# Kernel tuning notes

Measured on AMD Instinct MI355X. Metric: run time of the kernel, lower is better.

## Reference

```python
import jax, jax.numpy as jnp
import numpy as np

RADIUS = 5
KERNEL = 2 * RADIUS + 1  # 11
N_PATCHES = KERNEL * KERNEL  # 121
SIGMA_DIAG = np.array([10.0, 10.0, 0.02, 0.02, 0.02, 0.1, 0.1, 0.1], dtype=np.float32)


def _shift(x):
    # x: [B, C, H, W] -> [B, P, C, H, W] with P = KERNEL^2 reflect-padded window shifts
    b, c, h, w = x.shape
    xp = jnp.pad(x, ((0, 0), (0, 0), (RADIUS, RADIUS), (RADIUS, RADIUS)), mode='reflect')
    patches = [xp[:, :, dy:dy + h, dx:dx + w]
               for dy in range(KERNEL) for dx in range(KERNEL)]
    return jnp.stack(patches, axis=1)


def setup_inputs() -> dict:
    key = jax.random.key(0)
    k1, k2 = jax.random.split(key)
    image = jax.random.uniform(k1, (2, 3, 256, 256), dtype=jnp.float32)
    guidance = jax.random.uniform(k2, (2, 8, 256, 256), dtype=jnp.float32)
    return {"image": image, "guidance": guidance}


def reference(image, guidance):
    # sigma_inv = inverse of diag(SIGMA_DIAG): diagonal, so just reciprocal per channel
    sigma_inv = jnp.asarray(1.0 / SIGMA_DIAG, dtype=guidance.dtype)  # [8]

    sg = _shift(guidance)                       # [B, P, 8, H, W]
    center = sg[:, N_PATCHES // 2:N_PATCHES // 2 + 1]
    diff = sg - center                          # [B, P, 8, H, W]
    # Mahalanobis^2 with diagonal sigma_inv: sum_c diff^2 / sigma_c
    maha_sq = jnp.einsum('bpchw,c->bphw', diff * diff, sigma_inv)
    weights = jnp.exp(-0.5 * maha_sq)           # [B, P, H, W]

    si = _shift(image)                          # [B, P, 3, H, W]
    weighted_sum = jnp.einsum('bpchw,bphw->bchw', si, weights)
    sum_w = jnp.clip(jnp.sum(weights, axis=1, keepdims=False), 1e-10, None)  # [B, H, W]
    return weighted_sum / sum_w[:, None]        # [B, 3, H, W]
```

## Files before the change

### kernel.cpp

```cpp
#include <hip/hip_runtime.h>

#define RADIUS 5
#define TILEX  32
#define TILEY  16
#define HX     (TILEX + 2*RADIUS)
#define HY     (TILEY + 2*RADIUS)
#define HPITCH 22
#define H      256
#define W      256

#define KA (-0.072134752f)
#define KB (-36.06737602f)
#define KC (-7.213475204f)

typedef float v2f __attribute__((ext_vector_type(2)));

struct Center { v2f h01, h23, h45, h67; float phic; };

__device__ __forceinline__ void accum(const float4 A, const float4 G, const float4 P,
                                      const Center& C, const float pg,
                                      v2f& swx, v2f& syz) {
    v2f t2;  t2.x = P.w + pg; t2.y = 0.f;
    v2f a01; a01.x = A.x; a01.y = A.y;
    v2f a23; a23.x = A.z; a23.y = A.w;
    v2f g01; g01.x = G.x; g01.y = G.y;
    v2f g23; g23.x = G.z; g23.y = G.w;
    t2 = __builtin_elementwise_fma(C.h01, a01, t2);
    t2 = __builtin_elementwise_fma(C.h23, a23, t2);
    t2 = __builtin_elementwise_fma(C.h45, g01, t2);
    t2 = __builtin_elementwise_fma(C.h67, g23, t2);
    const float w = __builtin_amdgcn_exp2f(t2.x + t2.y);
    v2f w2;  w2.x = w;   w2.y = w;
    v2f m0;  m0.x = 1.f; m0.y = P.x;
    v2f m1;  m1.x = P.y; m1.y = P.z;
    swx = __builtin_elementwise_fma(w2, m0, swx);
    syz = __builtin_elementwise_fma(w2, m1, syz);
}

__global__ __launch_bounds__(512, 2) void jbf_kernel(
    const float* __restrict__ image,
    const float* __restrict__ guidance,
    float* __restrict__ out)
{
    __shared__ float4 g0e[HY * HPITCH], g0o[HY * HPITCH];
    __shared__ float4 g1e[HY * HPITCH], g1o[HY * HPITCH];
    __shared__ float4 ime[HY * HPITCH], imo[HY * HPITCH];

    const int id = blockIdx.x;
    const int c_xcd = id & 7;
    const int r_rnk = id >> 3;
    const int b       = c_xcd >> 2;
    const int tile_x0 = (((c_xcd & 3) << 1) | (r_rnk & 1)) * TILEX;
    const int tile_y0 = (r_rnk >> 1) * TILEY;

    const int txp = threadIdx.x;
    const int h   = threadIdx.y;
    const int typ = threadIdx.z;
    const int tid = (typ * 4 + h) * 16 + txp;

    const float* gbase = guidance + (size_t)b * 8 * H * W;
    const float* ibase = image    + (size_t)b * 3 * H * W;

    for (int idx = tid; idx < HX * HY; idx += 512) {
        const int ly = idx / HX;
        const int lx = idx - ly * HX;
        int gy = tile_y0 - RADIUS + ly;
        int gx = tile_x0 - RADIUS + lx;
        gy = (gy < 0) ? -gy : ((gy >= H) ? 2 * (H - 1) - gy : gy);
        gx = (gx < 0) ? -gx : ((gx >= W) ? 2 * (W - 1) - gx : gx);
        const int off = gy * W + gx;
        const int l   = ly * HPITCH + (lx >> 1);
        const float4 v0 = make_float4(gbase[0*H*W+off], gbase[1*H*W+off],
                                      gbase[2*H*W+off], gbase[3*H*W+off]);
        const float4 v1 = make_float4(gbase[4*H*W+off], gbase[5*H*W+off],
                                      gbase[6*H*W+off], gbase[7*H*W+off]);
        const float phi = KA * (v0.x*v0.x + v0.y*v0.y)
                        + KB * (v0.z*v0.z + v0.w*v0.w + v1.x*v1.x)
                        + KC * (v1.y*v1.y + v1.z*v1.z + v1.w*v1.w);
        const float4 vi = make_float4(ibase[0*H*W+off], ibase[1*H*W+off],
                                      ibase[2*H*W+off], phi);
        if (lx & 1) { g0o[l] = v0; g1o[l] = v1; imo[l] = vi; }
        else        { g0e[l] = v0; g1e[l] = v1; ime[l] = vi; }
    }
    __syncthreads();

    Center c[2][2];
    #pragma unroll
    for (int cy = 0; cy < 2; ++cy) {
        const int row = (2 * typ + 5 + cy) * HPITCH;
        #pragma unroll
        for (int cx = 0; cx < 2; ++cx) {
            const int ci = row + txp + 2 + cx;
            const float4 gA = cx ? g0e[ci] : g0o[ci];
            const float4 gB = cx ? g1e[ci] : g1o[ci];
            const float4 pv = cx ? ime[ci] : imo[ci];
            c[cx][cy].h01.x = -2.f*KA*gA.x;  c[cx][cy].h01.y = -2.f*KA*gA.y;
            c[cx][cy].h23.x = -2.f*KB*gA.z;  c[cx][cy].h23.y = -2.f*KB*gA.w;
            c[cx][cy].h45.x = -2.f*KB*gB.x;  c[cx][cy].h45.y = -2.f*KC*gB.y;
            c[cx][cy].h67.x = -2.f*KC*gB.z;  c[cx][cy].h67.y = -2.f*KC*gB.w;
            c[cx][cy].phic  = pv.w;
        }
    }

    v2f swx[2][2], syz[2][2];
    #pragma unroll
    for (int cx = 0; cx < 2; ++cx)
        #pragma unroll
        for (int cy = 0; cy < 2; ++cy) {
            swx[cx][cy].x = 0.f; swx[cx][cy].y = 0.f;
            syz[cx][cy].x = 0.f; syz[cx][cy].y = 0.f;
        }

    #pragma unroll
    for (int i = 0; i < 3; ++i) {
        const int r  = 4 * i + h;
        const int rb = (2 * typ + r) * HPITCH + txp;
        const float b0 = (r <= 10) ? 0.0f : -1000.0f;
        const float b1 = (r >= 1)  ? 0.0f : -1000.0f;
        const float pg00 = c[0][0].phic + b0, pg01 = c[0][1].phic + b1;
        const float pg10 = c[1][0].phic + b0, pg11 = c[1][1].phic + b1;
        #pragma unroll
        for (int k = 0; k <= 5; ++k) {
            {
                const float4 A = g0e[rb + k], G = g1e[rb + k], P = ime[rb + k];
                accum(A, G, P, c[0][0], pg00, swx[0][0], syz[0][0]);
                accum(A, G, P, c[0][1], pg01, swx[0][1], syz[0][1]);
                if (k >= 1) {
                    accum(A, G, P, c[1][0], pg10, swx[1][0], syz[1][0]);
                    accum(A, G, P, c[1][1], pg11, swx[1][1], syz[1][1]);
                }
            }
            {
                const float4 A = g0o[rb + k], G = g1o[rb + k], P = imo[rb + k];
                if (k <= 4) {
                    accum(A, G, P, c[0][0], pg00, swx[0][0], syz[0][0]);
                    accum(A, G, P, c[0][1], pg01, swx[0][1], syz[0][1]);
                }
                accum(A, G, P, c[1][0], pg10, swx[1][0], syz[1][0]);
                accum(A, G, P, c[1][1], pg11, swx[1][1], syz[1][1]);
            }
        }
    }

    #pragma unroll
    for (int cx = 0; cx < 2; ++cx)
        #pragma unroll
        for (int cy = 0; cy < 2; ++cy) {
            swx[cx][cy].x += __shfl_xor(swx[cx][cy].x, 16);
            swx[cx][cy].x += __shfl_xor(swx[cx][cy].x, 32);
            swx[cx][cy].y += __shfl_xor(swx[cx][cy].y, 16);
            swx[cx][cy].y += __shfl_xor(swx[cx][cy].y, 32);
            syz[cx][cy].x += __shfl_xor(syz[cx][cy].x, 16);
            syz[cx][cy].x += __shfl_xor(syz[cx][cy].x, 32);
            syz[cx][cy].y += __shfl_xor(syz[cx][cy].y, 16);
            syz[cx][cy].y += __shfl_xor(syz[cx][cy].y, 32);
        }

    if (h == 0) {
        const size_t base = (size_t)b * 3 * H * W
                          + (size_t)(tile_y0 + 2 * typ) * W + (tile_x0 + 2 * txp);
        #pragma unroll
        for (int cy = 0; cy < 2; ++cy) {
            const float i0 = 1.0f / swx[0][cy].x;
            const float i1 = 1.0f / swx[1][cy].x;
            float2* __restrict__ o2 = (float2*)(out + base + (size_t)cy * W);
            o2[0]           = make_float2(swx[0][cy].y * i0, swx[1][cy].y * i1);
            o2[(H*W) / 2]   = make_float2(syz[0][cy].x * i0, syz[1][cy].x * i1);
            o2[(2*H*W) / 2] = make_float2(syz[0][cy].y * i0, syz[1][cy].y * i1);
        }
    }
}

extern "C" void kernel_launch(void* const* d_in, const int* in_sizes, int n_in,
                              void* d_out, int out_size, void* d_ws, size_t ws_size,
                              hipStream_t stream) {
    const float* image    = (const float*)d_in[0];
    const float* guidance = (const float*)d_in[1];
    float* out            = (float*)d_out;

    dim3 grid(256, 1, 1);
    dim3 block(16, 4, 8);
    hipLaunchKernelGGL(jbf_kernel, grid, block, 0, stream, image, guidance, out);
}
```

Measured before the change: 66.91 us.

## Give each thread a 4x2 output block and split columns by parity across thread halves

```diff
diff --git a/kernel.cpp b/kernel.cpp
--- a/kernel.cpp
+++ b/kernel.cpp
@@ -5,7 +5,8 @@
 #define TILEY  16
 #define HX     (TILEX + 2*RADIUS)
 #define HY     (TILEY + 2*RADIUS)
-#define HPITCH 22
+#define HPITCH 23
+#define EO     (HY * HPITCH)
 #define H      256
 #define W      256
 
@@ -42,9 +43,9 @@
     const float* __restrict__ guidance,
     float* __restrict__ out)
 {
-    __shared__ float4 g0e[HY * HPITCH], g0o[HY * HPITCH];
-    __shared__ float4 g1e[HY * HPITCH], g1o[HY * HPITCH];
-    __shared__ float4 ime[HY * HPITCH], imo[HY * HPITCH];
+    __shared__ float4 g0[2 * EO];
+    __shared__ float4 g1[2 * EO];
+    __shared__ float4 im[2 * EO];
 
     const int id = blockIdx.x;
     const int c_xcd = id & 7;
@@ -54,9 +55,11 @@
     const int tile_y0 = (r_rnk >> 1) * TILEY;
 
     const int txp = threadIdx.x;
-    const int h   = threadIdx.y;
+    const int hy  = threadIdx.y;
+    const int h   = hy & 3;
+    const int ks  = hy >> 2;
     const int typ = threadIdx.z;
-    const int tid = (typ * 4 + h) * 16 + txp;
+    const int tid = (typ * 8 + hy) * 8 + txp;
 
     const float* gbase = guidance + (size_t)b * 8 * H * W;
     const float* ibase = image    + (size_t)b * 3 * H * W;
@@ -69,7 +72,7 @@
         gy = (gy < 0) ? -gy : ((gy >= H) ? 2 * (H - 1) - gy : gy);
         gx = (gx < 0) ? -gx : ((gx >= W) ? 2 * (W - 1) - gx : gx);
         const int off = gy * W + gx;
-        const int l   = ly * HPITCH + (lx >> 1);
+        const int l   = ly * HPITCH + (lx >> 1) + ((lx & 1) ? EO : 0);
         const float4 v0 = make_float4(gbase[0*H*W+off], gbase[1*H*W+off],
                                       gbase[2*H*W+off], gbase[3*H*W+off]);
         const float4 v1 = make_float4(gbase[4*H*W+off], gbase[5*H*W+off],
@@ -79,21 +82,20 @@
                         + KC * (v1.y*v1.y + v1.z*v1.z + v1.w*v1.w);
         const float4 vi = make_float4(ibase[0*H*W+off], ibase[1*H*W+off],
                                       ibase[2*H*W+off], phi);
-        if (lx & 1) { g0o[l] = v0; g1o[l] = v1; imo[l] = vi; }
-        else        { g0e[l] = v0; g1e[l] = v1; ime[l] = vi; }
+        g0[l] = v0; g1[l] = v1; im[l] = vi;
     }
     __syncthreads();
 
-    Center c[2][2];
+    Center c[4][2];
     #pragma unroll
     for (int cy = 0; cy < 2; ++cy) {
-        const int row = (2 * typ + 5 + cy) * HPITCH;
+        const int row = (2 * typ + 5 + cy) * HPITCH + 2 * txp;
+        const int ci[4] = { row + 2 + EO, row + 3, row + 3 + EO, row + 4 };
         #pragma unroll
-        for (int cx = 0; cx < 2; ++cx) {
-            const int ci = row + txp + 2 + cx;
-            const float4 gA = cx ? g0e[ci] : g0o[ci];
-            const float4 gB = cx ? g1e[ci] : g1o[ci];
-            const float4 pv = cx ? ime[ci] : imo[ci];
+        for (int cx = 0; cx < 4; ++cx) {
+            const float4 gA = g0[ci[cx]];
+            const float4 gB = g1[ci[cx]];
+            const float4 pv = im[ci[cx]];
             c[cx][cy].h01.x = -2.f*KA*gA.x;  c[cx][cy].h01.y = -2.f*KA*gA.y;
             c[cx][cy].h23.x = -2.f*KB*gA.z;  c[cx][cy].h23.y = -2.f*KB*gA.w;
             c[cx][cy].h45.x = -2.f*KB*gB.x;  c[cx][cy].h45.y = -2.f*KC*gB.y;
@@ -102,71 +104,79 @@
         }
     }
 
-    v2f swx[2][2], syz[2][2];
+    v2f swx[4][2], syz[4][2];
     #pragma unroll
-    for (int cx = 0; cx < 2; ++cx)
+    for (int cx = 0; cx < 4; ++cx)
         #pragma unroll
         for (int cy = 0; cy < 2; ++cy) {
             swx[cx][cy].x = 0.f; swx[cx][cy].y = 0.f;
             syz[cx][cy].x = 0.f; syz[cx][cy].y = 0.f;
         }
 
+    const float bE = ks ? -1000.f : 0.f;
+    const float bO = ks ? 0.f : -1000.f;
+    const int   pb = ks * EO;
+
     #pragma unroll
     for (int i = 0; i < 3; ++i) {
         const int r  = 4 * i + h;
-        const int rb = (2 * typ + r) * HPITCH + txp;
+        const int rb = (2 * typ + r) * HPITCH + 2 * txp + pb;
         const float b0 = (r <= 10) ? 0.0f : -1000.0f;
         const float b1 = (r >= 1)  ? 0.0f : -1000.0f;
-        const float pg00 = c[0][0].phic + b0, pg01 = c[0][1].phic + b1;
-        const float pg10 = c[1][0].phic + b0, pg11 = c[1][1].phic + b1;
+        float pgp[4][2], pgb[4][2];
         #pragma unroll
-        for (int k = 0; k <= 5; ++k) {
-            {
-                const float4 A = g0e[rb + k], G = g1e[rb + k], P = ime[rb + k];
-                accum(A, G, P, c[0][0], pg00, swx[0][0], syz[0][0]);
-                accum(A, G, P, c[0][1], pg01, swx[0][1], syz[0][1]);
-                if (k >= 1) {
-                    accum(A, G, P, c[1][0], pg10, swx[1][0], syz[1][0]);
-                    accum(A, G, P, c[1][1], pg11, swx[1][1], syz[1][1]);
-                }
-            }
-            {
-                const float4 A = g0o[rb + k], G = g1o[rb + k], P = imo[rb + k];
-                if (k <= 4) {
-                    accum(A, G, P, c[0][0], pg00, swx[0][0], syz[0][0]);
-                    accum(A, G, P, c[0][1], pg01, swx[0][1], syz[0][1]);
-                }
-                accum(A, G, P, c[1][0], pg10, swx[1][0], syz[1][0]);
-                accum(A, G, P, c[1][1], pg11, swx[1][1], syz[1][1]);
-            }
+        for (int cx = 0; cx < 4; ++cx) {
+            pgp[cx][0] = c[cx][0].phic + b0;
+            pgp[cx][1] = c[cx][1].phic + b1;
+            const float bx = (cx & 1) ? bO : bE;
+            pgb[cx][0] = pgp[cx][0] + bx;
+            pgb[cx][1] = pgp[cx][1] + bx;
         }
+        #define ACCP(cx) do { \
+            accum(A, G, P, c[cx][0], pgp[cx][0], swx[cx][0], syz[cx][0]); \
+            accum(A, G, P, c[cx][1], pgp[cx][1], swx[cx][1], syz[cx][1]); } while (0)
+        #define ACCB(cx) do { \
+            accum(A, G, P, c[cx][0], pgb[cx][0], swx[cx][0], syz[cx][0]); \
+            accum(A, G, P, c[cx][1], pgb[cx][1], swx[cx][1], syz[cx][1]); } while (0)
+        #pragma unroll
+        for (int k = 0; k < 7; ++k) {
+            const float4 A = g0[rb + k], G = g1[rb + k], P = im[rb + k];
+            if (k == 0)      { ACCP(0); ACCB(1); }
+            else if (k == 1) { ACCP(0); ACCP(1); ACCP(2); ACCB(3); }
+            else if (k <= 4) { ACCP(0); ACCP(1); ACCP(2); ACCP(3); }
+            else if (k == 5) { ACCB(0); ACCP(1); ACCP(2); ACCP(3); }
+            else             { ACCB(2); ACCP(3); }
+        }
+        #undef ACCP
+        #undef ACCB
     }
 
+    #define RED(v) do { v += __shfl_xor(v, 8); v += __shfl_xor(v, 16); \
+                        v += __shfl_xor(v, 32); } while (0)
     #pragma unroll
-    for (int cx = 0; cx < 2; ++cx)
+    for (int cx = 0; cx < 4; ++cx)
         #pragma unroll
         for (int cy = 0; cy < 2; ++cy) {
-            swx[cx][cy].x += __shfl_xor(swx[cx][cy].x, 16);
-            swx[cx][cy].x += __shfl_xor(swx[cx][cy].x, 32);
-            swx[cx][cy].y += __shfl_xor(swx[cx][cy].y, 16);
-            swx[cx][cy].y += __shfl_xor(swx[cx][cy].y, 32);
-            syz[cx][cy].x += __shfl_xor(syz[cx][cy].x, 16);
-            syz[cx][cy].x += __shfl_xor(syz[cx][cy].x, 32);
-            syz[cx][cy].y += __shfl_xor(syz[cx][cy].y, 16);
-            syz[cx][cy].y += __shfl_xor(syz[cx][cy].y, 32);
+            RED(swx[cx][cy].x);  RED(swx[cx][cy].y);
+            RED(syz[cx][cy].x);  RED(syz[cx][cy].y);
         }
+    #undef RED
 
-    if (h == 0) {
+    if (hy == 0) {
         const size_t base = (size_t)b * 3 * H * W
-                          + (size_t)(tile_y0 + 2 * typ) * W + (tile_x0 + 2 * txp);
+                          + (size_t)(tile_y0 + 2 * typ) * W + (tile_x0 + 4 * txp);
         #pragma unroll
         for (int cy = 0; cy < 2; ++cy) {
-            const float i0 = 1.0f / swx[0][cy].x;
-            const float i1 = 1.0f / swx[1][cy].x;
-            float2* __restrict__ o2 = (float2*)(out + base + (size_t)cy * W);
-            o2[0]           = make_float2(swx[0][cy].y * i0, swx[1][cy].y * i1);
-            o2[(H*W) / 2]   = make_float2(syz[0][cy].x * i0, syz[1][cy].x * i1);
-            o2[(2*H*W) / 2] = make_float2(syz[0][cy].y * i0, syz[1][cy].y * i1);
+            float inv[4];
+            #pragma unroll
+            for (int cx = 0; cx < 4; ++cx) inv[cx] = 1.0f / swx[cx][cy].x;
+            float4* __restrict__ o4 = (float4*)(out + base + (size_t)cy * W);
+            o4[0]             = make_float4(swx[0][cy].y*inv[0], swx[1][cy].y*inv[1],
+                                            swx[2][cy].y*inv[2], swx[3][cy].y*inv[3]);
+            o4[(H*W) / 4]     = make_float4(syz[0][cy].x*inv[0], syz[1][cy].x*inv[1],
+                                            syz[2][cy].x*inv[2], syz[3][cy].x*inv[3]);
+            o4[(2*H*W) / 4]   = make_float4(syz[0][cy].y*inv[0], syz[1][cy].y*inv[1],
+                                            syz[2][cy].y*inv[2], syz[3][cy].y*inv[3]);
         }
     }
 }
@@ -179,6 +189,6 @@
     float* out            = (float*)d_out;
 
     dim3 grid(256, 1, 1);
-    dim3 block(16, 4, 8);
+    dim3 block(8, 8, 8);
     hipLaunchKernelGGL(jbf_kernel, grid, block, 0, stream, image, guidance, out);
 }
```

Measured after the change: 69.08 us. +3.3%, slower.
